# Optimization experiments

Hardware: AMD Instinct MI355X
Metric: run time of the kernel (lower is better)

## Reference

```python
import jax, jax.numpy as jnp
import numpy as np

N_NODES = 50000
N_EDGES = 600000
IN_DIM = 128
HID = 64
HEADS = 4
OUT_DIM = 64
EPS = 1e-5


def setup_inputs() -> dict:
    key = jax.random.key(0)
    ks = jax.random.split(key, 20)
    s = 0.05
    inp = {
        "x": jax.random.normal(ks[0], (N_NODES, IN_DIM), jnp.float32),
        "edge_index": jax.random.randint(ks[1], (2, N_EDGES), 0, N_NODES, jnp.int32),
        "drift_weight": jax.random.uniform(ks[2], (1,), jnp.float32),
        # GAT layer 1: in_dim -> heads*hid, concat
        "W1": jax.random.normal(ks[3], (IN_DIM, HEADS * HID), jnp.float32) * s,
        "a_src1": jax.random.normal(ks[4], (HEADS, HID), jnp.float32) * s,
        "a_dst1": jax.random.normal(ks[5], (HEADS, HID), jnp.float32) * s,
        "b1": jnp.zeros((HEADS * HID,), jnp.float32),
        # BatchNorm over heads*hid features
        "gamma": jnp.ones((HEADS * HID,), jnp.float32),
        "beta": jnp.zeros((HEADS * HID,), jnp.float32),
        # GAT layer 2: heads*hid -> hid, mean over heads
        "W2": jax.random.normal(ks[6], (HEADS * HID, HEADS * HID), jnp.float32) * s,
        "a_src2": jax.random.normal(ks[7], (HEADS, HID), jnp.float32) * s,
        "a_dst2": jax.random.normal(ks[8], (HEADS, HID), jnp.float32) * s,
        "b2": jnp.zeros((HID,), jnp.float32),
        # GCN layers
        "Wg1": jax.random.normal(ks[9], (IN_DIM, HID), jnp.float32) * s,
        "bg1": jnp.zeros((HID,), jnp.float32),
        "Wg2": jax.random.normal(ks[10], (HID, OUT_DIM), jnp.float32) * s,
        "bg2": jnp.zeros((OUT_DIM,), jnp.float32),
    }
    return inp


def _gat_layer(x, src, dst, W, a_src, a_dst, b, concat):
    # PyG GATConv (dropout disabled at eval): h = xW; e_ij = LeakyReLU(a_src.h_j + a_dst.h_i)
    # softmax over incoming edges of each dst node; out_i = sum_j alpha_ij h_j
    n = x.shape[0]
    H, C = a_src.shape
    h = (x @ W).reshape(n, H, C)                      # [N,H,C]
    e = jax.nn.leaky_relu(
        (h * a_src).sum(-1)[src] + (h * a_dst).sum(-1)[dst], 0.2
    )                                                 # [E,H]
    m = jax.ops.segment_max(e, dst, num_segments=n)
    p = jnp.exp(e - m[dst])
    z = jax.ops.segment_sum(p, dst, num_segments=n)
    alpha = p / z[dst]                                # [E,H]
    out = jax.ops.segment_sum(h[src] * alpha[:, :, None], dst, num_segments=n)
    out = out.reshape(n, H * C) if concat else out.mean(axis=1)
    return out + b


def _gcn_layer(x, src, dst, W, b):
    n = x.shape[0]
    deg = jax.ops.segment_sum(jnp.ones(src.shape[0], x.dtype), dst, num_segments=n)
    dinv = jax.lax.rsqrt(jnp.maximum(deg, 1.0))
    h = x @ W
    norm = (dinv[src] * dinv[dst])[:, None]           # [E,1]
    return jax.ops.segment_sum(h[src] * norm, dst, num_segments=n) + b


def _batchnorm(x, gamma, beta):
    mu = x.mean(axis=0)
    var = x.var(axis=0)
    return (x - mu) * jax.lax.rsqrt(var + EPS) * gamma + beta


def reference(x, edge_index, drift_weight, W1, a_src1, a_dst1, b1, gamma, beta,
              W2, a_src2, a_dst2, b2, Wg1, bg1, Wg2, bg2):
    n = x.shape[0]
    loop = jnp.arange(n, dtype=edge_index.dtype)
    src = jnp.concatenate([edge_index[0], loop])
    dst = jnp.concatenate([edge_index[1], loop])

    # GAT branch
    h = _gat_layer(x, src, dst, W1, a_src1, a_dst1, b1, concat=True)
    h = jax.nn.elu(_batchnorm(h, gamma, beta))
    h_gat = _gat_layer(h, src, dst, W2, a_src2, a_dst2, b2, concat=False)  # [N,HID]

    # GCN branch
    g = jax.nn.relu(_gcn_layer(x, src, dst, Wg1, bg1))
    h_gcn = _gcn_layer(g, src, dst, Wg2, bg2)                              # [N,OUT]

    # drift-weighted fusion
    w = drift_weight[0]
    return w * h_gat + (1.0 - w) * h_gcn
```

## Files before the change

kernel.cpp:

```cpp
#include <hip/hip_runtime.h>

#define N_NODES 50000
#define M_PAD   50048
#define N_EDGES 600000
#define ETOT    650000
#define EPS     1e-5f
#define SCAN_BLOCKS 196

typedef short bf16x8 __attribute__((ext_vector_type(8)));
typedef float f32x4  __attribute__((ext_vector_type(4)));

static __device__ __forceinline__ float leaky(float v) { return v >= 0.f ? v : 0.2f * v; }

static __device__ __forceinline__ ushort f2bf(float f) {
  unsigned u = __float_as_uint(f);
  return (ushort)((u + 0x7fff + ((u >> 16) & 1)) >> 16);
}
static __device__ __forceinline__ float bf2f(ushort u) {
  return __uint_as_float(((unsigned)u) << 16);
}

template <int K, bool OUTBF>
__global__ __launch_bounds__(256) void gemm_bf16(
    const ushort* __restrict__ A, const ushort* __restrict__ Bt,
    void* __restrict__ C, int M, int Nfull) {
  __shared__ char As[64 * 128];
  __shared__ char Bs[64 * 128];
  const int tid = threadIdx.x;
  const int w = tid >> 6, lane = tid & 63;
  const int wr = w >> 1, wc = w & 1;
  const int m0 = blockIdx.x * 64, n0 = blockIdx.y * 64;

  f32x4 acc[2][2] = {};

  for (int k0 = 0; k0 < K; k0 += 64) {
    __syncthreads();
#pragma unroll
    for (int j = 0; j < 2; ++j) {
      int i = tid + j * 256;
      int row = i >> 3;
      int cb = (i & 7) * 16;
      int dst = row * 128 + (cb ^ ((row & 7) << 4));
      uint4 va = *(const uint4*)((const char*)A + ((size_t)(m0 + row) * K + k0) * 2 + cb);
      *(uint4*)(As + dst) = va;
      uint4 vb = *(const uint4*)((const char*)Bt + ((size_t)(n0 + row) * K + k0) * 2 + cb);
      *(uint4*)(Bs + dst) = vb;
    }
    __syncthreads();
#pragma unroll
    for (int c = 0; c < 2; ++c) {
      bf16x8 af[2], bfr[2];
      int kb = (lane >> 4) * 16 + c * 64;
#pragma unroll
      for (int m = 0; m < 2; ++m) {
        int lr = wr * 32 + m * 16 + (lane & 15);
        af[m] = *(const bf16x8*)(As + lr * 128 + (kb ^ ((lr & 7) << 4)));
      }
#pragma unroll
      for (int n = 0; n < 2; ++n) {
        int lr = wc * 32 + n * 16 + (lane & 15);
        bfr[n] = *(const bf16x8*)(Bs + lr * 128 + (kb ^ ((lr & 7) << 4)));
      }
#pragma unroll
      for (int m = 0; m < 2; ++m)
#pragma unroll
        for (int n = 0; n < 2; ++n)
          acc[m][n] = __builtin_amdgcn_mfma_f32_16x16x32_bf16(af[m], bfr[n], acc[m][n], 0, 0, 0);
    }
  }
#pragma unroll
  for (int m = 0; m < 2; ++m)
#pragma unroll
    for (int n = 0; n < 2; ++n)
#pragma unroll
      for (int i = 0; i < 4; ++i) {
        int row = m0 + wr * 32 + m * 16 + (lane >> 4) * 4 + i;
        int col = n0 + wc * 32 + n * 16 + (lane & 15);
        if (row < M) {
          if (OUTBF) ((ushort*)C)[(size_t)row * Nfull + col] = f2bf(acc[m][n][i]);
          else       ((float*)C)[(size_t)row * Nfull + col] = acc[m][n][i];
        }
      }
}

__global__ __launch_bounds__(256) void cast_x_bf16(const float* __restrict__ x, ushort* __restrict__ o) {
  int i = blockIdx.x * 256 + threadIdx.x;
  if (i >= M_PAD * 32) return;
  int i4 = i * 4;
  int row = i4 >> 7;
  ushort4 r;
  if (row < N_NODES) {
    const float4 v = *(const float4*)(x + i4);
    r.x = f2bf(v.x); r.y = f2bf(v.y); r.z = f2bf(v.z); r.w = f2bf(v.w);
  } else {
    r.x = r.y = r.z = r.w = 0;
  }
  *(ushort4*)(o + i4) = r;
}

__global__ __launch_bounds__(256) void tcast_w(const float* __restrict__ W, ushort* __restrict__ Wt,
                                               int K, int N) {
  int i = blockIdx.x * 256 + threadIdx.x;
  if (i >= K * N) return;
  int k = i / N, n = i - k * N;
  Wt[n * K + k] = f2bf(W[i]);
}

__global__ __launch_bounds__(256) void attn_scores_bf(
    const ushort* __restrict__ h, const float* __restrict__ a_src,
    const float* __restrict__ a_dst, float* __restrict__ ssrc, float* __restrict__ sdst) {
  const int wave = threadIdx.x >> 6, lane = threadIdx.x & 63;
  const int row = blockIdx.x * 4 + wave;
  if (row >= N_NODES) return;
  const ushort4 hv = *(const ushort4*)(h + (size_t)row * 256 + lane * 4);
  float h0 = bf2f(hv.x), h1 = bf2f(hv.y), h2 = bf2f(hv.z), h3 = bf2f(hv.w);
  const float4 as = *(const float4*)(a_src + lane * 4);
  const float4 ad = *(const float4*)(a_dst + lane * 4);
  float ps = h0 * as.x + h1 * as.y + h2 * as.z + h3 * as.w;
  float pd = h0 * ad.x + h1 * ad.y + h2 * ad.z + h3 * ad.w;
#pragma unroll
  for (int off = 1; off < 16; off <<= 1) {
    ps += __shfl_xor(ps, off);
    pd += __shfl_xor(pd, off);
  }
  if ((lane & 15) == 0) {
    int hh = lane >> 4;
    ssrc[row * 4 + hh] = ps;
    sdst[row * 4 + hh] = pd;
  }
}

static __device__ __forceinline__ void edge_sd(const int* ei, int e, int& src, int& dst) {
  if (e < N_EDGES) { src = ei[e]; dst = ei[N_EDGES + e]; }
  else             { src = dst = e - N_EDGES; }
}

__global__ __launch_bounds__(256) void deg_count_int(const int* __restrict__ ei, int* __restrict__ degi) {
  int e = blockIdx.x * 256 + threadIdx.x;
  if (e >= ETOT) return;
  int dst = (e < N_EDGES) ? ei[N_EDGES + e] : (e - N_EDGES);
  atomicAdd(&degi[dst], 1);
}

__global__ __launch_bounds__(256) void scan1(const int* __restrict__ degi,
                                             int* __restrict__ partial, int* __restrict__ bsum) {
  __shared__ int sm[256];
  int i = blockIdx.x * 256 + threadIdx.x;
  int v = (i < N_NODES) ? degi[i] : 0;
  sm[threadIdx.x] = v;
  __syncthreads();
#pragma unroll
  for (int off = 1; off < 256; off <<= 1) {
    int t = (threadIdx.x >= off) ? sm[threadIdx.x - off] : 0;
    __syncthreads();
    sm[threadIdx.x] += t;
    __syncthreads();
  }
  if (i < N_NODES) partial[i] = sm[threadIdx.x] - v;
  if (threadIdx.x == 255) bsum[blockIdx.x] = sm[255];
}

__global__ __launch_bounds__(256) void scan2(int* __restrict__ bsum) {
  __shared__ int sm[256];
  int v = (threadIdx.x < SCAN_BLOCKS) ? bsum[threadIdx.x] : 0;
  sm[threadIdx.x] = v;
  __syncthreads();
#pragma unroll
  for (int off = 1; off < 256; off <<= 1) {
    int t = (threadIdx.x >= off) ? sm[threadIdx.x - off] : 0;
    __syncthreads();
    sm[threadIdx.x] += t;
    __syncthreads();
  }
  if (threadIdx.x < SCAN_BLOCKS) bsum[threadIdx.x] = sm[threadIdx.x] - v;
}

__global__ __launch_bounds__(256) void scan3(int* __restrict__ rowstart, const int* __restrict__ bsum,
                                             int* __restrict__ cursor, const int* __restrict__ degi,
                                             float* __restrict__ dinv) {
  int i = blockIdx.x * 256 + threadIdx.x;
  if (i >= N_NODES) return;
  int r = rowstart[i] + bsum[blockIdx.x];
  rowstart[i] = r;
  cursor[i] = r;
  dinv[i] = rsqrtf(fmaxf((float)degi[i], 1.0f));
}

__global__ __launch_bounds__(256) void scatter_k(const int* __restrict__ ei,
                                                 int* __restrict__ cursor, int* __restrict__ csr) {
  int e = blockIdx.x * 256 + threadIdx.x;
  if (e >= ETOT) return;
  int src, dst; edge_sd(ei, e, src, dst);
  int pos = atomicAdd(&cursor[dst], 1);
  csr[pos] = src;
}

__global__ __launch_bounds__(256) void gat_agg1_bf(
    const int* __restrict__ rowstart, const int* __restrict__ degi, const int* __restrict__ csr,
    const ushort* __restrict__ h, const float* __restrict__ ssrc, const float* __restrict__ sdst,
    float* __restrict__ outp) {
  int dst = blockIdx.x * 4 + (threadIdx.x >> 6);
  if (dst >= N_NODES) return;
  int lane = threadIdx.x & 63;
  int hh = lane >> 4;
  int rs = rowstart[dst], re = rs + degi[dst];
  float sd = sdst[dst * 4 + hh];
  float z = 0.f;
  float ax = 0.f, ay = 0.f, az = 0.f, aw = 0.f;
  for (int j = rs; j < re; ++j) {
    int src = csr[j];
    float p = __expf(leaky(ssrc[src * 4 + hh] + sd));
    z += p;
    const ushort4 hv = *(const ushort4*)(h + (size_t)src * 256 + lane * 4);
    ax += p * bf2f(hv.x); ay += p * bf2f(hv.y); az += p * bf2f(hv.z); aw += p * bf2f(hv.w);
  }
  float inv = 1.f / z;
  float4 o = { ax * inv, ay * inv, az * inv, aw * inv };
  *(float4*)(outp + (size_t)dst * 256 + lane * 4) = o;
}

__global__ __launch_bounds__(256) void gat_agg2_bf(
    const int* __restrict__ rowstart, const int* __restrict__ degi, const int* __restrict__ csr,
    const ushort* __restrict__ h2, const float* __restrict__ ssrc, const float* __restrict__ sdst,
    float* __restrict__ outp) {
  int dst = blockIdx.x * 4 + (threadIdx.x >> 6);
  if (dst >= N_NODES) return;
  int lane = threadIdx.x & 63;
  int rs = rowstart[dst], re = rs + degi[dst];
  const float4 sd = *(const float4*)(sdst + dst * 4);
  float z0 = 0.f, z1 = 0.f, z2 = 0.f, z3 = 0.f;
  float a0 = 0.f, a1 = 0.f, a2 = 0.f, a3 = 0.f;
  for (int j = rs; j < re; ++j) {
    int src = csr[j];
    const float4 ss = *(const float4*)(ssrc + src * 4);
    float p0 = __expf(leaky(ss.x + sd.x));
    float p1 = __expf(leaky(ss.y + sd.y));
    float p2 = __expf(leaky(ss.z + sd.z));
    float p3 = __expf(leaky(ss.w + sd.w));
    z0 += p0; z1 += p1; z2 += p2; z3 += p3;
    const ushort* hb = h2 + (size_t)src * 256;
    a0 += p0 * bf2f(hb[lane]);
    a1 += p1 * bf2f(hb[64 + lane]);
    a2 += p2 * bf2f(hb[128 + lane]);
    a3 += p3 * bf2f(hb[192 + lane]);
  }
  outp[(size_t)dst * 64 + lane] = 0.25f * (a0 / z0 + a1 / z1 + a2 / z2 + a3 / z3);
}

__global__ __launch_bounds__(256) void gcn_agg_relu_bf(
    const int* __restrict__ rowstart, const int* __restrict__ degi, const int* __restrict__ csr,
    const ushort* __restrict__ g, const float* __restrict__ dinv, const float* __restrict__ bias,
    ushort* __restrict__ outp) {
  int dst = blockIdx.x * 4 + (threadIdx.x >> 6);
  if (dst >= N_NODES) return;
  int lane = threadIdx.x & 63;
  int rs = rowstart[dst], re = rs + degi[dst];
  float acc = 0.f;
  for (int j = rs; j < re; ++j) {
    int src = csr[j];
    acc += dinv[src] * bf2f(g[(size_t)src * 64 + lane]);
  }
  float v = acc * dinv[dst] + bias[lane];
  outp[(size_t)dst * 64 + lane] = f2bf(fmaxf(v, 0.f));
}

__global__ __launch_bounds__(256) void gcn_agg_fuse_bf(
    const int* __restrict__ rowstart, const int* __restrict__ degi, const int* __restrict__ csr,
    const ushort* __restrict__ g2, const float* __restrict__ dinv, const float* __restrict__ bg2,
    const float* __restrict__ hgat, const float* __restrict__ b2, const float* __restrict__ dw,
    float* __restrict__ outp) {
  int dst = blockIdx.x * 4 + (threadIdx.x >> 6);
  if (dst >= N_NODES) return;
  int lane = threadIdx.x & 63;
  int rs = rowstart[dst], re = rs + degi[dst];
  float acc = 0.f;
  for (int j = rs; j < re; ++j) {
    int src = csr[j];
    acc += dinv[src] * bf2f(g2[(size_t)src * 64 + lane]);
  }
  float w = dw[0];
  float gcn = acc * dinv[dst] + bg2[lane];
  float gat = hgat[(size_t)dst * 64 + lane] + b2[lane];
  outp[(size_t)dst * 64 + lane] = w * gat + (1.f - w) * gcn;
}

__global__ __launch_bounds__(256) void bn_stats(
    const float* __restrict__ x, float* __restrict__ sum, float* __restrict__ sumsq) {
  int f = threadIdx.x;
  int r0 = blockIdx.x * 64;
  int rend = min(r0 + 64, N_NODES);
  float s = 0.f, s2 = 0.f;
  for (int r = r0; r < rend; ++r) {
    float v = x[(size_t)r * 256 + f];
    s += v; s2 += v * v;
  }
  atomicAdd(&sum[f], s);
  atomicAdd(&sumsq[f], s2);
}

__global__ __launch_bounds__(256) void bn_apply_bf16(
    const float* __restrict__ x, const float* __restrict__ sum, const float* __restrict__ sumsq,
    const float* __restrict__ gamma, const float* __restrict__ beta, ushort* __restrict__ o) {
  size_t i = (size_t)blockIdx.x * 256 + threadIdx.x;
  if (i >= (size_t)N_NODES * 256) return;
  int f = (int)(i & 255);
  const float invN = 1.0f / N_NODES;
  float mu = sum[f] * invN;
  float var = sumsq[f] * invN - mu * mu;
  float v = (x[i] - mu) * rsqrtf(var + EPS) * gamma[f] + beta[f];
  float e = v > 0.f ? v : expf(v) - 1.0f;
  o[i] = f2bf(e);
}

extern "C" void kernel_launch(void* const* d_in, const int* in_sizes, int n_in,
                              void* d_out, int out_size, void* d_ws, size_t ws_size,
                              hipStream_t stream) {
  const float* x     = (const float*)d_in[0];
  const int*   ei    = (const int*)d_in[1];
  const float* dw    = (const float*)d_in[2];
  const float* W1    = (const float*)d_in[3];
  const float* as1   = (const float*)d_in[4];
  const float* ad1   = (const float*)d_in[5];
  const float* gamma = (const float*)d_in[7];
  const float* beta  = (const float*)d_in[8];
  const float* W2    = (const float*)d_in[9];
  const float* as2   = (const float*)d_in[10];
  const float* ad2   = (const float*)d_in[11];
  const float* b2    = (const float*)d_in[12];
  const float* Wg1   = (const float*)d_in[13];
  const float* bg1   = (const float*)d_in[14];
  const float* Wg2   = (const float*)d_in[15];
  const float* bg2   = (const float*)d_in[16];
  float* out = (float*)d_out;

  char* p = (char*)d_ws;
  size_t off = 0;
  auto alloc = [&](size_t bytes) {
    char* r = p + off;
    off = (off + bytes + 255) & ~(size_t)255;
    return r;
  };
  float*  bufB  = (float*)alloc((size_t)N_NODES * 256 * 4);
  float*  bufC  = (float*)alloc((size_t)N_NODES * 64 * 4);
  ushort* xbf   = (ushort*)alloc((size_t)M_PAD * 128 * 2);
  ushort* R1    = (ushort*)alloc((size_t)M_PAD * 256 * 2);
  ushort* g1bf  = (ushort*)alloc((size_t)N_NODES * 64 * 2);
  ushort* gbf   = (ushort*)alloc((size_t)M_PAD * 64 * 2);
  ushort* g2bf  = (ushort*)alloc((size_t)N_NODES * 64 * 2);
  ushort* w1t   = (ushort*)alloc((size_t)256 * 128 * 2);
  ushort* w2t   = (ushort*)alloc((size_t)256 * 256 * 2);
  ushort* wg1t  = (ushort*)alloc((size_t)64 * 128 * 2);
  ushort* wg2t  = (ushort*)alloc((size_t)64 * 64 * 2);
  float*  ssrc1 = (float*)alloc((size_t)N_NODES * 4 * 4);
  float*  sdst1 = (float*)alloc((size_t)N_NODES * 4 * 4);
  float*  ssrc2 = (float*)alloc((size_t)N_NODES * 4 * 4);
  float*  sdst2 = (float*)alloc((size_t)N_NODES * 4 * 4);
  int*    degi  = (int*)alloc((size_t)N_NODES * 4);
  int*    rowst = (int*)alloc((size_t)N_NODES * 4);
  int*    cursor= (int*)alloc((size_t)N_NODES * 4);
  int*    bsum  = (int*)alloc(SCAN_BLOCKS * 4);
  float*  dinv  = (float*)alloc((size_t)N_NODES * 4);
  int*    csr   = (int*)alloc((size_t)ETOT * 4);
  float*  bnsum = (float*)alloc(256 * 4);
  float*  bnsq  = (float*)alloc(256 * 4);
  ushort* h2bf  = (ushort*)bufB;

  const dim3 blk(256);
  const int egrid = (ETOT + 255) / 256;
  const int ngrid = 12500;

  hipMemsetAsync(degi, 0, (size_t)N_NODES * 4, stream);
  hipMemsetAsync(bnsum, 0, 256 * 4, stream);
  hipMemsetAsync(bnsq, 0, 256 * 4, stream);
  hipMemsetAsync(R1 + (size_t)N_NODES * 256, 0, (size_t)(M_PAD - N_NODES) * 256 * 2, stream);
  hipMemsetAsync(gbf + (size_t)N_NODES * 64, 0, (size_t)(M_PAD - N_NODES) * 64 * 2, stream);

  deg_count_int<<<egrid, blk, 0, stream>>>(ei, degi);
  scan1<<<SCAN_BLOCKS, blk, 0, stream>>>(degi, rowst, bsum);
  scan2<<<1, blk, 0, stream>>>(bsum);
  scan3<<<SCAN_BLOCKS, blk, 0, stream>>>(rowst, bsum, cursor, degi, dinv);
  scatter_k<<<egrid, blk, 0, stream>>>(ei, cursor, csr);
  cast_x_bf16<<<(M_PAD * 32 + 255) / 256, blk, 0, stream>>>(x, xbf);
  tcast_w<<<(128 * 256 + 255) / 256, blk, 0, stream>>>(W1, w1t, 128, 256);
  tcast_w<<<(256 * 256 + 255) / 256, blk, 0, stream>>>(W2, w2t, 256, 256);
  tcast_w<<<(128 * 64 + 255) / 256, blk, 0, stream>>>(Wg1, wg1t, 128, 64);
  tcast_w<<<(64 * 64 + 255) / 256, blk, 0, stream>>>(Wg2, wg2t, 64, 64);

  gemm_bf16<128, true><<<dim3(782, 4), blk, 0, stream>>>(xbf, w1t, R1, N_NODES, 256);
  gemm_bf16<128, true><<<dim3(782, 1), blk, 0, stream>>>(xbf, wg1t, g1bf, N_NODES, 64);

  attn_scores_bf<<<ngrid, blk, 0, stream>>>(R1, as1, ad1, ssrc1, sdst1);
  gat_agg1_bf<<<ngrid, blk, 0, stream>>>(rowst, degi, csr, R1, ssrc1, sdst1, bufB);

  gcn_agg_relu_bf<<<ngrid, blk, 0, stream>>>(rowst, degi, csr, g1bf, dinv, bg1, gbf);
  gemm_bf16<64, true><<<dim3(782, 1), blk, 0, stream>>>(gbf, wg2t, g2bf, N_NODES, 64);

  bn_stats<<<(N_NODES + 63) / 64, blk, 0, stream>>>(bufB, bnsum, bnsq);
  bn_apply_bf16<<<(int)(((size_t)N_NODES * 256 + 255) / 256), blk, 0, stream>>>(
      bufB, bnsum, bnsq, gamma, beta, R1);

  gemm_bf16<256, true><<<dim3(782, 4), blk, 0, stream>>>(R1, w2t, h2bf, N_NODES, 256);
  attn_scores_bf<<<ngrid, blk, 0, stream>>>(h2bf, as2, ad2, ssrc2, sdst2);
  gat_agg2_bf<<<ngrid, blk, 0, stream>>>(rowst, degi, csr, h2bf, ssrc2, sdst2, bufC);

  gcn_agg_fuse_bf<<<ngrid, blk, 0, stream>>>(rowst, degi, csr, g2bf, dinv, bg2, bufC, b2, dw, out);
}
```

Baseline: 602.8 us.

## Interleave GAT layer-2 heads in GEMM output and unroll edge gather loops by two

The second GAT GEMM now writes its output with head-interleaved columns, so each lane reads its four heads' values for one channel with a single 8-byte load instead of four scattered 2-byte loads. A matching attention-score kernel and aggregation kernel are added for the permuted layout. All four CSR aggregation loops are also unrolled by two so that two neighbour gathers are in flight at once. The trade-offs are extra register use and 2-byte scattered stores in the GEMM epilogue.

```diff
diff --git a/kernel.cpp b/kernel.cpp
--- a/kernel.cpp
+++ b/kernel.cpp
@@ -20,7 +20,7 @@
   return __uint_as_float(((unsigned)u) << 16);
 }
 
-template <int K, bool OUTBF>
+template <int K, bool OUTBF, bool PERM>
 __global__ __launch_bounds__(256) void gemm_bf16(
     const ushort* __restrict__ A, const ushort* __restrict__ Bt,
     void* __restrict__ C, int M, int Nfull) {
@@ -77,8 +77,12 @@
         int row = m0 + wr * 32 + m * 16 + (lane >> 4) * 4 + i;
         int col = n0 + wc * 32 + n * 16 + (lane & 15);
         if (row < M) {
-          if (OUTBF) ((ushort*)C)[(size_t)row * Nfull + col] = f2bf(acc[m][n][i]);
-          else       ((float*)C)[(size_t)row * Nfull + col] = acc[m][n][i];
+          if (OUTBF) {
+            int oc = PERM ? (((col & 63) << 2) | (col >> 6)) : col;
+            ((ushort*)C)[(size_t)row * Nfull + oc] = f2bf(acc[m][n][i]);
+          } else {
+            ((float*)C)[(size_t)row * Nfull + col] = acc[m][n][i];
+          }
         }
       }
 }
@@ -130,6 +134,33 @@
   }
 }
 
+__global__ __launch_bounds__(256) void attn_scores_perm(
+    const ushort* __restrict__ hp, const float* __restrict__ a_src,
+    const float* __restrict__ a_dst, float* __restrict__ ssrc, float* __restrict__ sdst) {
+  const int wave = threadIdx.x >> 6, lane = threadIdx.x & 63;
+  const int row = blockIdx.x * 4 + wave;
+  if (row >= N_NODES) return;
+  const ushort4 hv = *(const ushort4*)(hp + (size_t)row * 256 + lane * 4);
+  float h0 = bf2f(hv.x), h1 = bf2f(hv.y), h2 = bf2f(hv.z), h3 = bf2f(hv.w);
+  float s0 = h0 * a_src[lane],       d0 = h0 * a_dst[lane];
+  float s1 = h1 * a_src[64 + lane],  d1 = h1 * a_dst[64 + lane];
+  float s2 = h2 * a_src[128 + lane], d2 = h2 * a_dst[128 + lane];
+  float s3 = h3 * a_src[192 + lane], d3 = h3 * a_dst[192 + lane];
+#pragma unroll
+  for (int off = 1; off < 64; off <<= 1) {
+    s0 += __shfl_xor(s0, off); d0 += __shfl_xor(d0, off);
+    s1 += __shfl_xor(s1, off); d1 += __shfl_xor(d1, off);
+    s2 += __shfl_xor(s2, off); d2 += __shfl_xor(d2, off);
+    s3 += __shfl_xor(s3, off); d3 += __shfl_xor(d3, off);
+  }
+  if (lane == 0) {
+    float4 sv = { s0, s1, s2, s3 };
+    float4 dv = { d0, d1, d2, d3 };
+    *(float4*)(ssrc + row * 4) = sv;
+    *(float4*)(sdst + row * 4) = dv;
+  }
+}
+
 static __device__ __forceinline__ void edge_sd(const int* ei, int e, int& src, int& dst) {
   if (e < N_EDGES) { src = ei[e]; dst = ei[N_EDGES + e]; }
   else             { src = dst = e - N_EDGES; }
@@ -207,21 +238,36 @@
   float sd = sdst[dst * 4 + hh];
   float z = 0.f;
   float ax = 0.f, ay = 0.f, az = 0.f, aw = 0.f;
-  for (int j = rs; j < re; ++j) {
-    int src = csr[j];
-    float p = __expf(leaky(ssrc[src * 4 + hh] + sd));
-    z += p;
-    const ushort4 hv = *(const ushort4*)(h + (size_t)src * 256 + lane * 4);
-    ax += p * bf2f(hv.x); ay += p * bf2f(hv.y); az += p * bf2f(hv.z); aw += p * bf2f(hv.w);
+  int j = rs;
+  for (; j + 1 < re; j += 2) {
+    int s0 = csr[j], s1 = csr[j + 1];
+    float e0 = ssrc[s0 * 4 + hh], e1 = ssrc[s1 * 4 + hh];
+    const ushort4 hv0 = *(const ushort4*)(h + (size_t)s0 * 256 + lane * 4);
+    const ushort4 hv1 = *(const ushort4*)(h + (size_t)s1 * 256 + lane * 4);
+    float p0 = __expf(leaky(e0 + sd));
+    float p1 = __expf(leaky(e1 + sd));
+    z += p0 + p1;
+    ax += p0 * bf2f(hv0.x) + p1 * bf2f(hv1.x);
+    ay += p0 * bf2f(hv0.y) + p1 * bf2f(hv1.y);
+    az += p0 * bf2f(hv0.z) + p1 * bf2f(hv1.z);
+    aw += p0 * bf2f(hv0.w) + p1 * bf2f(hv1.w);
+  }
+  if (j < re) {
+    int s0 = csr[j];
+    float p0 = __expf(leaky(ssrc[s0 * 4 + hh] + sd));
+    const ushort4 hv0 = *(const ushort4*)(h + (size_t)s0 * 256 + lane * 4);
+    z += p0;
+    ax += p0 * bf2f(hv0.x); ay += p0 * bf2f(hv0.y);
+    az += p0 * bf2f(hv0.z); aw += p0 * bf2f(hv0.w);
   }
   float inv = 1.f / z;
   float4 o = { ax * inv, ay * inv, az * inv, aw * inv };
   *(float4*)(outp + (size_t)dst * 256 + lane * 4) = o;
 }
 
-__global__ __launch_bounds__(256) void gat_agg2_bf(
+__global__ __launch_bounds__(256) void gat_agg2_perm(
     const int* __restrict__ rowstart, const int* __restrict__ degi, const int* __restrict__ csr,
-    const ushort* __restrict__ h2, const float* __restrict__ ssrc, const float* __restrict__ sdst,
+    const ushort* __restrict__ hp, const float* __restrict__ ssrc, const float* __restrict__ sdst,
     float* __restrict__ outp) {
   int dst = blockIdx.x * 4 + (threadIdx.x >> 6);
   if (dst >= N_NODES) return;
@@ -230,19 +276,34 @@
   const float4 sd = *(const float4*)(sdst + dst * 4);
   float z0 = 0.f, z1 = 0.f, z2 = 0.f, z3 = 0.f;
   float a0 = 0.f, a1 = 0.f, a2 = 0.f, a3 = 0.f;
-  for (int j = rs; j < re; ++j) {
-    int src = csr[j];
-    const float4 ss = *(const float4*)(ssrc + src * 4);
-    float p0 = __expf(leaky(ss.x + sd.x));
-    float p1 = __expf(leaky(ss.y + sd.y));
-    float p2 = __expf(leaky(ss.z + sd.z));
-    float p3 = __expf(leaky(ss.w + sd.w));
-    z0 += p0; z1 += p1; z2 += p2; z3 += p3;
-    const ushort* hb = h2 + (size_t)src * 256;
-    a0 += p0 * bf2f(hb[lane]);
-    a1 += p1 * bf2f(hb[64 + lane]);
-    a2 += p2 * bf2f(hb[128 + lane]);
-    a3 += p3 * bf2f(hb[192 + lane]);
+  int j = rs;
+  for (; j + 1 < re; j += 2) {
+    int s0 = csr[j], s1 = csr[j + 1];
+    const float4 ss0 = *(const float4*)(ssrc + s0 * 4);
+    const float4 ss1 = *(const float4*)(ssrc + s1 * 4);
+    const ushort4 hv0 = *(const ushort4*)(hp + (size_t)s0 * 256 + lane * 4);
+    const ushort4 hv1 = *(const ushort4*)(hp + (size_t)s1 * 256 + lane * 4);
+    float p00 = __expf(leaky(ss0.x + sd.x)), p10 = __expf(leaky(ss1.x + sd.x));
+    float p01 = __expf(leaky(ss0.y + sd.y)), p11 = __expf(leaky(ss1.y + sd.y));
+    float p02 = __expf(leaky(ss0.z + sd.z)), p12 = __expf(leaky(ss1.z + sd.z));
+    float p03 = __expf(leaky(ss0.w + sd.w)), p13 = __expf(leaky(ss1.w + sd.w));
+    z0 += p00 + p10; z1 += p01 + p11; z2 += p02 + p12; z3 += p03 + p13;
+    a0 += p00 * bf2f(hv0.x) + p10 * bf2f(hv1.x);
+    a1 += p01 * bf2f(hv0.y) + p11 * bf2f(hv1.y);
+    a2 += p02 * bf2f(hv0.z) + p12 * bf2f(hv1.z);
+    a3 += p03 * bf2f(hv0.w) + p13 * bf2f(hv1.w);
+  }
+  if (j < re) {
+    int s0 = csr[j];
+    const float4 ss0 = *(const float4*)(ssrc + s0 * 4);
+    const ushort4 hv0 = *(const ushort4*)(hp + (size_t)s0 * 256 + lane * 4);
+    float p00 = __expf(leaky(ss0.x + sd.x));
+    float p01 = __expf(leaky(ss0.y + sd.y));
+    float p02 = __expf(leaky(ss0.z + sd.z));
+    float p03 = __expf(leaky(ss0.w + sd.w));
+    z0 += p00; z1 += p01; z2 += p02; z3 += p03;
+    a0 += p00 * bf2f(hv0.x); a1 += p01 * bf2f(hv0.y);
+    a2 += p02 * bf2f(hv0.z); a3 += p03 * bf2f(hv0.w);
   }
   outp[(size_t)dst * 64 + lane] = 0.25f * (a0 / z0 + a1 / z1 + a2 / z2 + a3 / z3);
 }
@@ -256,9 +317,17 @@
   int lane = threadIdx.x & 63;
   int rs = rowstart[dst], re = rs + degi[dst];
   float acc = 0.f;
-  for (int j = rs; j < re; ++j) {
-    int src = csr[j];
-    acc += dinv[src] * bf2f(g[(size_t)src * 64 + lane]);
+  int j = rs;
+  for (; j + 1 < re; j += 2) {
+    int s0 = csr[j], s1 = csr[j + 1];
+    float d0 = dinv[s0], d1 = dinv[s1];
+    float v0 = bf2f(g[(size_t)s0 * 64 + lane]);
+    float v1 = bf2f(g[(size_t)s1 * 64 + lane]);
+    acc += d0 * v0 + d1 * v1;
+  }
+  if (j < re) {
+    int s0 = csr[j];
+    acc += dinv[s0] * bf2f(g[(size_t)s0 * 64 + lane]);
   }
   float v = acc * dinv[dst] + bias[lane];
   outp[(size_t)dst * 64 + lane] = f2bf(fmaxf(v, 0.f));
@@ -274,9 +343,17 @@
   int lane = threadIdx.x & 63;
   int rs = rowstart[dst], re = rs + degi[dst];
   float acc = 0.f;
-  for (int j = rs; j < re; ++j) {
-    int src = csr[j];
-    acc += dinv[src] * bf2f(g2[(size_t)src * 64 + lane]);
+  int j = rs;
+  for (; j + 1 < re; j += 2) {
+    int s0 = csr[j], s1 = csr[j + 1];
+    float d0 = dinv[s0], d1 = dinv[s1];
+    float v0 = bf2f(g2[(size_t)s0 * 64 + lane]);
+    float v1 = bf2f(g2[(size_t)s1 * 64 + lane]);
+    acc += d0 * v0 + d1 * v1;
+  }
+  if (j < re) {
+    int s0 = csr[j];
+    acc += dinv[s0] * bf2f(g2[(size_t)s0 * 64 + lane]);
   }
   float w = dw[0];
   float gcn = acc * dinv[dst] + bg2[lane];
@@ -363,7 +440,7 @@
   int*    csr   = (int*)alloc((size_t)ETOT * 4);
   float*  bnsum = (float*)alloc(256 * 4);
   float*  bnsq  = (float*)alloc(256 * 4);
-  ushort* h2bf  = (ushort*)bufB;
+  ushort* h2p   = (ushort*)bufB;
 
   const dim3 blk(256);
   const int egrid = (ETOT + 255) / 256;
@@ -386,22 +463,22 @@
   tcast_w<<<(128 * 64 + 255) / 256, blk, 0, stream>>>(Wg1, wg1t, 128, 64);
   tcast_w<<<(64 * 64 + 255) / 256, blk, 0, stream>>>(Wg2, wg2t, 64, 64);
 
-  gemm_bf16<128, true><<<dim3(782, 4), blk, 0, stream>>>(xbf, w1t, R1, N_NODES, 256);
-  gemm_bf16<128, true><<<dim3(782, 1), blk, 0, stream>>>(xbf, wg1t, g1bf, N_NODES, 64);
+  gemm_bf16<128, true, false><<<dim3(782, 4), blk, 0, stream>>>(xbf, w1t, R1, N_NODES, 256);
+  gemm_bf16<128, true, false><<<dim3(782, 1), blk, 0, stream>>>(xbf, wg1t, g1bf, N_NODES, 64);
 
   attn_scores_bf<<<ngrid, blk, 0, stream>>>(R1, as1, ad1, ssrc1, sdst1);
   gat_agg1_bf<<<ngrid, blk, 0, stream>>>(rowst, degi, csr, R1, ssrc1, sdst1, bufB);
 
   gcn_agg_relu_bf<<<ngrid, blk, 0, stream>>>(rowst, degi, csr, g1bf, dinv, bg1, gbf);
-  gemm_bf16<64, true><<<dim3(782, 1), blk, 0, stream>>>(gbf, wg2t, g2bf, N_NODES, 64);
+  gemm_bf16<64, true, false><<<dim3(782, 1), blk, 0, stream>>>(gbf, wg2t, g2bf, N_NODES, 64);
 
   bn_stats<<<(N_NODES + 63) / 64, blk, 0, stream>>>(bufB, bnsum, bnsq);
   bn_apply_bf16<<<(int)(((size_t)N_NODES * 256 + 255) / 256), blk, 0, stream>>>(
       bufB, bnsum, bnsq, gamma, beta, R1);
 
-  gemm_bf16<256, true><<<dim3(782, 4), blk, 0, stream>>>(R1, w2t, h2bf, N_NODES, 256);
-  attn_scores_bf<<<ngrid, blk, 0, stream>>>(h2bf, as2, ad2, ssrc2, sdst2);
-  gat_agg2_bf<<<ngrid, blk, 0, stream>>>(rowst, degi, csr, h2bf, ssrc2, sdst2, bufC);
+  gemm_bf16<256, true, true><<<dim3(782, 4), blk, 0, stream>>>(R1, w2t, h2p, N_NODES, 256);
+  attn_scores_perm<<<ngrid, blk, 0, stream>>>(h2p, as2, ad2, ssrc2, sdst2);
+  gat_agg2_perm<<<ngrid, blk, 0, stream>>>(rowst, degi, csr, h2p, ssrc2, sdst2, bufC);
 
   gcn_agg_fuse_bf<<<ngrid, blk, 0, stream>>>(rowst, degi, csr, g2bf, dinv, bg2, bufC, b2, dw, out);
 }
```

Result: faster. 559.9 us (-7.1%).
